# Kernel optimization log

Hardware: AMD Instinct MI355X
Metric: run time of the kernel (lower is better)

Reference implementation:

```python
import jax, jax.numpy as jnp
import numpy as np

L, C, F, K = 8192, 2048, 128, 257  # timesteps, input_size, filter_size, lag (odd => symmetric 'same' pad)
NY = 256  # number of overwritten channel rows


def setup_inputs() -> dict:
    key = jax.random.key(0)
    k1, k2, k3, k4 = jax.random.split(key, 4)
    x = jax.random.normal(k1, (L, C), dtype=jnp.float32)
    Yt = jax.random.randint(k2, (NY,), 0, C)
    # learned parameters (torch.rand -> uniform[0,1))
    g = jax.random.uniform(k3, (C, F), dtype=jnp.float32)
    kernel = jax.random.uniform(k4, (F, K), dtype=jnp.float32)
    return {"x": x, "Yt": Yt, "g": g, "kernel": kernel}


def reference(x, Yt, g, kernel):
    # synapse[c] is the per-channel 1D filter; the original builds a dense
    # (C, C, K) kernel whose only non-zero slices are the diagonal, so the
    # full conv1d is mathematically a depthwise (grouped) conv.
    synapse = jnp.matmul(g, kernel)          # (C, K)
    lhs = x.T[None]                          # (1, C, L)  NCH
    rhs = synapse[:, None, :]                # (C, 1, K)  OIH, groups=C
    pad = (kernel.shape[1] - 1) // 2         # torch padding='same', odd K
    out = jax.lax.conv_general_dilated(
        lhs, rhs,
        window_strides=(1,),
        padding=[(pad, pad)],
        feature_group_count=x.shape[1],
        dimension_numbers=("NCH", "OIH", "NCH"),
    )                                        # (1, C, L)
    # result[:, Yt, :] = x.T[Yt] : scatter-overwrite selected channel rows
    out = out.at[:, Yt, :].set(x.T[Yt][None])
    return out
```

## Files before the change

kernel.cpp:

```cpp
#include <hip/hip_runtime.h>

#define LL   8192
#define CC   2048
#define FF   128
#define KK   257
#define PAD  128

#define SROWP 328
#define NT   18
#define NCH  8
#define NW   8
#define ROWS 1288

typedef __bf16 bf16x8 __attribute__((ext_vector_type(8)));
typedef float  f32x16 __attribute__((ext_vector_type(16)));

static __device__ __forceinline__ unsigned short f2bf(float f) {
    unsigned u = __float_as_uint(f);
    u = (u + 0x7fffu + ((u >> 16) & 1u)) >> 16;
    return (unsigned short)u;
}

__global__ __launch_bounds__(256) void synb_kernel(const float* __restrict__ g,
                                                   const float* __restrict__ kern,
                                                   const int* __restrict__ Yt, int ny,
                                                   unsigned short* __restrict__ synEb) {
    __shared__ int sfl[4];
    const int c0 = blockIdx.x * 4;
    const int t  = threadIdx.x;
    if (t < 4) sfl[t] = 0;
    __syncthreads();
    for (int i = t; i < ny; i += 256) {
        int y = Yt[i];
        #pragma unroll
        for (int ii = 0; ii < 4; ++ii) if (y == c0 + ii) sfl[ii] = 1;
    }
    __syncthreads();
    const float* g0 = g + (size_t)(c0 + 0) * FF;
    const float* g1 = g + (size_t)(c0 + 1) * FF;
    const float* g2 = g + (size_t)(c0 + 2) * FF;
    const float* g3 = g + (size_t)(c0 + 3) * FF;
    const int fl0 = sfl[0], fl1 = sfl[1], fl2 = sfl[2], fl3 = sfl[3];
    for (int p = t; p < SROWP; p += 256) {
        const int kk = p - 32;
        float a0 = 0.f, a1 = 0.f, a2 = 0.f, a3 = 0.f;
        const bool inr = (kk >= 0) && (kk < KK);
        if (inr) {
            #pragma unroll 8
            for (int f = 0; f < FF; ++f) {
                float kv = kern[f * KK + kk];
                a0 += kv * g0[f];
                a1 += kv * g1[f];
                a2 += kv * g2[f];
                a3 += kv * g3[f];
            }
        }
        float dlt = (kk == PAD) ? 1.f : 0.f;
        float v0 = inr ? (fl0 ? dlt : a0) : 0.f;
        float v1 = inr ? (fl1 ? dlt : a1) : 0.f;
        float v2 = inr ? (fl2 ? dlt : a2) : 0.f;
        float v3 = inr ? (fl3 ? dlt : a3) : 0.f;
        synEb[(size_t)(c0 + 0) * SROWP + p] = f2bf(v0);
        synEb[(size_t)(c0 + 1) * SROWP + p] = f2bf(v1);
        synEb[(size_t)(c0 + 2) * SROWP + p] = f2bf(v2);
        synEb[(size_t)(c0 + 3) * SROWP + p] = f2bf(v3);
    }
}

static __device__ __forceinline__ void stage_issue(const float* __restrict__ x,
                                                   int W0, int c0, int t,
                                                   float2* ev, float2* ov) {
    #pragma unroll
    for (int k = 0; k < 5; ++k) {
        int pidx = (k << 9) + t;
        int ch2  = pidx & 3;
        int pp   = pidx >> 2;
        int lg   = W0 + (pp << 1) - 128;
        const float* sp = x + (size_t)lg * CC + c0 + (ch2 << 1);
        float2 a = make_float2(0.f, 0.f);
        float2 b = make_float2(0.f, 0.f);
        if ((unsigned)lg       < (unsigned)LL) a = *(const float2*)sp;
        if ((unsigned)(lg + 1) < (unsigned)LL) b = *(const float2*)(sp + CC);
        ev[k] = a; ov[k] = b;
    }
}

static __device__ __forceinline__ void stage_write(unsigned short (*buf)[ROWS], int t,
                                                   const float2* ev, const float2* ov) {
    #pragma unroll
    for (int k = 0; k < 5; ++k) {
        int pidx = (k << 9) + t;
        int ch2  = pidx & 3;
        int pp   = pidx >> 2;
        int gq   = pp >> 2;
        int gp   = gq ^ ((gq >> 3) & 7);
        int dw   = (gp << 2) | (pp & 3);
        const float* pe = (const float*)&ev[k];
        const float* po = (const float*)&ov[k];
        #pragma unroll
        for (int c2 = 0; c2 < 2; ++c2) {
            unsigned val = (unsigned)f2bf(pe[c2]) | ((unsigned)f2bf(po[c2]) << 16);
            ((unsigned*)buf[(ch2 << 1) + c2])[dw] = val;
        }
    }
}

__global__ __launch_bounds__(512, 2) void fused_conv(const float* __restrict__ x,
                                                     const unsigned short* __restrict__ synEb,
                                                     float* __restrict__ out) {
    __shared__ alignas(16) unsigned short xch[2][NCH][ROWS];
    __shared__ alignas(16) unsigned short synL[NCH][SROWP];
    const int t = threadIdx.x;

    const int d  = blockIdx.x;
    const int cg = ((d & 7) << 5) | (d >> 3);
    const int c0 = cg << 3;

    const int ci = t >> 6;
    const int ln = t & 63;
    const int j = ln & 31, q = ln >> 5;
    const int bb  = (q << 4) - 2 * j + 64;
    const int dwb = bb >> 2;
    const int sh  = (bb & 2) << 3;
    const int gb  = (j << 2) + q;

    float2 ev[5], ov[5];
    stage_issue(x, 0, c0, t, ev, ov);

    for (int u = t; u < NCH * (SROWP / 2); u += 512) {
        int rr = u / (SROWP / 2), uu = u - rr * (SROWP / 2);
        ((unsigned*)synL[rr])[uu] =
            ((const unsigned*)(synEb + (size_t)(c0 + rr) * SROWP))[uu];
    }
    __syncthreads();

    bf16x8 bfrag[NT];
    {
        const unsigned* rp = (const unsigned*)(synL[ci]) + dwb;
        #pragma unroll
        for (int m = 0; m < NT; ++m) {
            unsigned w0 = rp[(m << 3) + 0], w1 = rp[(m << 3) + 1], w2 = rp[(m << 3) + 2],
                     w3 = rp[(m << 3) + 3], w4 = rp[(m << 3) + 4];
            union { unsigned dd[4]; bf16x8 v; } B;
            B.dd[0] = (unsigned)((((unsigned long long)w1 << 32) | w0) >> sh);
            B.dd[1] = (unsigned)((((unsigned long long)w2 << 32) | w1) >> sh);
            B.dd[2] = (unsigned)((((unsigned long long)w3 << 32) | w2) >> sh);
            B.dd[3] = (unsigned)((((unsigned long long)w4 << 32) | w3) >> sh);
            bfrag[m] = B.v;
        }
    }

    int aoff[NT];
    #pragma unroll
    for (int m = 0; m < NT; ++m) {
        int gq2 = gb + (m << 1);
        int gp2 = gq2 ^ ((gq2 >> 3) & 7);
        aoff[m] = gp2 << 4;
    }

    stage_write(xch[0], t, ev, ov);
    __syncthreads();

    for (int w = 0; w < NW; ++w) {
        const int cur = w & 1;
        const int W0  = w << 10;
        if (w + 1 < NW) stage_issue(x, W0 + 1024, c0, t, ev, ov);

        const char* xrow = (const char*)xch[cur][ci];
        f32x16 acc;
        #pragma unroll
        for (int r = 0; r < 16; ++r) acc[r] = 0.f;
        #pragma unroll
        for (int m = 0; m < NT; ++m) {
            union { int4 i4; bf16x8 v; } A;
            A.i4 = *(const int4*)(xrow + aoff[m]);
            acc = __builtin_amdgcn_mfma_f32_32x32x16_bf16(A.v, bfrag[m], acc, 0, 0, 0);
        }
        float* o = out + (size_t)(c0 + ci) * LL + W0 + j;
        #pragma unroll
        for (int r = 0; r < 16; ++r) {
            int row = (r & 3) + ((r >> 2) << 3) + (q << 2);
            o[row << 5] = acc[r];
        }
        __syncthreads();
        if (w + 1 < NW) stage_write(xch[cur ^ 1], t, ev, ov);
        __syncthreads();
    }
}

extern "C" void kernel_launch(void* const* d_in, const int* in_sizes, int n_in,
                              void* d_out, int out_size, void* d_ws, size_t ws_size,
                              hipStream_t stream) {
    const float* x    = (const float*)d_in[0];
    const int*   Yt   = (const int*)  d_in[1];
    const float* g    = (const float*)d_in[2];
    const float* kern = (const float*)d_in[3];
    float* out = (float*)d_out;
    const int ny = in_sizes[1];

    unsigned short* synEb = (unsigned short*)d_ws;

    synb_kernel<<<CC / 4, 256, 0, stream>>>(g, kern, Yt, ny, synEb);
    fused_conv<<<256, 512, 0, stream>>>(x, synEb, out);
}
```

Baseline: 155.3 us.

## Split conv across more blocks and store pre-shifted filter copies in LDS

Each block now covers 4 channels and half the time axis, with 256 threads instead of 512. The launch grows to 1024 blocks and the occupancy hint to 4 blocks per CU. The filter is kept in LDS as two copies offset by one element, so each lane reads aligned B fragments directly inside the MFMA loop. This replaces the register-cached fragments built with 64-bit funnel shifts. The change aims for better load balance and occupancy, at the cost of extra LDS reads per MFMA, overlapping halo loads at the time split, and more per-block setup.

```diff
diff --git a/kernel.cpp b/kernel.cpp
--- a/kernel.cpp
+++ b/kernel.cpp
@@ -8,8 +8,8 @@
 
 #define SROWP 328
 #define NT   18
-#define NCH  8
-#define NW   8
+#define NCH  4
+#define NW   4
 #define ROWS 1288
 
 typedef __bf16 bf16x8 __attribute__((ext_vector_type(8)));
@@ -72,9 +72,9 @@
                                                    float2* ev, float2* ov) {
     #pragma unroll
     for (int k = 0; k < 5; ++k) {
-        int pidx = (k << 9) + t;
-        int ch2  = pidx & 3;
-        int pp   = pidx >> 2;
+        int pidx = (k << 8) + t;
+        int ch2  = pidx & 1;
+        int pp   = pidx >> 1;
         int lg   = W0 + (pp << 1) - 128;
         const float* sp = x + (size_t)lg * CC + c0 + (ch2 << 1);
         float2 a = make_float2(0.f, 0.f);
@@ -89,9 +89,9 @@
                                                    const float2* ev, const float2* ov) {
     #pragma unroll
     for (int k = 0; k < 5; ++k) {
-        int pidx = (k << 9) + t;
-        int ch2  = pidx & 3;
-        int pp   = pidx >> 2;
+        int pidx = (k << 8) + t;
+        int ch2  = pidx & 1;
+        int pp   = pidx >> 1;
         int gq   = pp >> 2;
         int gp   = gq ^ ((gq >> 3) & 7);
         int dw   = (gp << 2) | (pp & 3);
@@ -105,65 +105,47 @@
     }
 }
 
-__global__ __launch_bounds__(512, 2) void fused_conv(const float* __restrict__ x,
+__global__ __launch_bounds__(256, 4) void fused_conv(const float* __restrict__ x,
                                                      const unsigned short* __restrict__ synEb,
                                                      float* __restrict__ out) {
     __shared__ alignas(16) unsigned short xch[2][NCH][ROWS];
-    __shared__ alignas(16) unsigned short synL[NCH][SROWP];
+    __shared__ alignas(16) unsigned short synD[NCH][2][SROWP];
     const int t = threadIdx.x;
 
     const int d  = blockIdx.x;
-    const int cg = ((d & 7) << 5) | (d >> 3);
-    const int c0 = cg << 3;
+    const int cg = ((d & 7) << 6) | (d >> 4);
+    const int c0 = cg << 2;
+    const int L0 = ((d >> 3) & 1) << 12;
 
     const int ci = t >> 6;
     const int ln = t & 63;
     const int j = ln & 31, q = ln >> 5;
-    const int bb  = (q << 4) - 2 * j + 64;
-    const int dwb = bb >> 2;
-    const int sh  = (bb & 2) << 3;
-    const int gb  = (j << 2) + q;
+    const int gb = (j << 2) + q;
+    const int ib   = (q << 3) - j + 32;
+    const int ppar = ib & 1;
+    const int e0   = (ib - ppar) >> 1;
 
     float2 ev[5], ov[5];
-    stage_issue(x, 0, c0, t, ev, ov);
+    stage_issue(x, L0, c0, t, ev, ov);
 
-    for (int u = t; u < NCH * (SROWP / 2); u += 512) {
-        int rr = u / (SROWP / 2), uu = u - rr * (SROWP / 2);
-        ((unsigned*)synL[rr])[uu] =
-            ((const unsigned*)(synEb + (size_t)(c0 + rr) * SROWP))[uu];
-    }
-    __syncthreads();
-
-    bf16x8 bfrag[NT];
-    {
-        const unsigned* rp = (const unsigned*)(synL[ci]) + dwb;
-        #pragma unroll
-        for (int m = 0; m < NT; ++m) {
-            unsigned w0 = rp[(m << 3) + 0], w1 = rp[(m << 3) + 1], w2 = rp[(m << 3) + 2],
-                     w3 = rp[(m << 3) + 3], w4 = rp[(m << 3) + 4];
-            union { unsigned dd[4]; bf16x8 v; } B;
-            B.dd[0] = (unsigned)((((unsigned long long)w1 << 32) | w0) >> sh);
-            B.dd[1] = (unsigned)((((unsigned long long)w2 << 32) | w1) >> sh);
-            B.dd[2] = (unsigned)((((unsigned long long)w3 << 32) | w2) >> sh);
-            B.dd[3] = (unsigned)((((unsigned long long)w4 << 32) | w3) >> sh);
-            bfrag[m] = B.v;
-        }
-    }
-
-    int aoff[NT];
-    #pragma unroll
-    for (int m = 0; m < NT; ++m) {
-        int gq2 = gb + (m << 1);
-        int gp2 = gq2 ^ ((gq2 >> 3) & 7);
-        aoff[m] = gp2 << 4;
+    for (int u = t; u < NCH * 2 * SROWP; u += 256) {
+        int ci2 = u / (2 * SROWP);
+        int rem = u - ci2 * (2 * SROWP);
+        int p   = (rem >= SROWP) ? 1 : 0;
+        int idx = rem - (p ? SROWP : 0);
+        int src = idx + p;
+        if (src > SROWP - 1) src = SROWP - 1;
+        synD[ci2][p][idx] = synEb[(size_t)(c0 + ci2) * SROWP + src];
     }
 
     stage_write(xch[0], t, ev, ov);
     __syncthreads();
 
+    const unsigned* bp = (const unsigned*)(synD[ci][ppar]) + e0;
+
     for (int w = 0; w < NW; ++w) {
         const int cur = w & 1;
-        const int W0  = w << 10;
+        const int W0  = L0 + (w << 10);
         if (w + 1 < NW) stage_issue(x, W0 + 1024, c0, t, ev, ov);
 
         const char* xrow = (const char*)xch[cur][ci];
@@ -172,9 +154,16 @@
         for (int r = 0; r < 16; ++r) acc[r] = 0.f;
         #pragma unroll
         for (int m = 0; m < NT; ++m) {
+            int gq2 = gb + (m << 1);
+            int gp2 = gq2 ^ ((gq2 >> 3) & 7);
             union { int4 i4; bf16x8 v; } A;
-            A.i4 = *(const int4*)(xrow + aoff[m]);
-            acc = __builtin_amdgcn_mfma_f32_32x32x16_bf16(A.v, bfrag[m], acc, 0, 0, 0);
+            A.i4 = *(const int4*)(xrow + (gp2 << 4));
+            union { unsigned dd[4]; bf16x8 v; } B;
+            B.dd[0] = bp[(m << 3) + 0];
+            B.dd[1] = bp[(m << 3) + 1];
+            B.dd[2] = bp[(m << 3) + 2];
+            B.dd[3] = bp[(m << 3) + 3];
+            acc = __builtin_amdgcn_mfma_f32_32x32x16_bf16(A.v, B.v, acc, 0, 0, 0);
         }
         float* o = out + (size_t)(c0 + ci) * LL + W0 + j;
         #pragma unroll
@@ -201,5 +190,5 @@
     unsigned short* synEb = (unsigned short*)d_ws;
 
     synb_kernel<<<CC / 4, 256, 0, stream>>>(g, kern, Yt, ny, synEb);
-    fused_conv<<<256, 512, 0, stream>>>(x, synEb, out);
+    fused_conv<<<1024, 256, 0, stream>>>(x, synEb, out);
 }
```

New measurement: 164.8 us. 1.06x slower.
